# Kernel tuning notes

Hardware: AMD Instinct MI355X
Metric: run time of the kernel (lower is better)

Reference implementation:

```python
import jax, jax.numpy as jnp
import numpy as np

USER_NUM = 100000
ITEM_NUM = 50000
N_NODES = USER_NUM + ITEM_NUM
NNZ = 4800000
EMB = 64
N_LAYERS = 3
EPS = 0.2
NORM_EPS = 1e-12  # matches torch F.normalize eps clamp


def setup_inputs() -> dict:
    key = jax.random.key(0)
    ks = jax.random.split(key, 6)
    user_emb = jax.random.normal(ks[0], (USER_NUM, EMB), dtype=jnp.float32)
    item_emb = jax.random.normal(ks[1], (ITEM_NUM, EMB), dtype=jnp.float32)
    adj_rows = jax.random.randint(ks[2], (NNZ,), 0, N_NODES, dtype=jnp.int32)
    adj_cols = jax.random.randint(ks[3], (NNZ,), 0, N_NODES, dtype=jnp.int32)
    adj_vals = jax.random.uniform(ks[4], (NNZ,), dtype=jnp.float32)
    noise = jax.random.uniform(ks[5], (N_LAYERS, N_NODES, EMB), dtype=jnp.float32)
    return {"user_emb": user_emb, "item_emb": item_emb, "adj_rows": adj_rows,
            "adj_cols": adj_cols, "adj_vals": adj_vals, "noise": noise}


def reference(user_emb, item_emb, adj_rows, adj_cols, adj_vals, noise):
    # ego: [N, d]
    ego = jnp.concatenate([user_emb, item_emb], axis=0)

    def spmm(x):
        # sparse_norm_adj @ x via COO gather + segment-sum scatter
        return jax.ops.segment_sum(adj_vals[:, None] * x[adj_cols], adj_rows,
                                   num_segments=N_NODES)

    layer_outs = []
    for k in range(N_LAYERS):
        ego = spmm(ego)
        # perturbed=True branch: ego += sign(ego) * l2_normalize(noise) * eps
        r = noise[k]
        r_unit = r / jnp.maximum(jnp.linalg.norm(r, axis=-1, keepdims=True), NORM_EPS)
        ego = ego + jnp.sign(ego) * r_unit * EPS
        layer_outs.append(ego)

    all_emb = jnp.mean(jnp.stack(layer_outs, axis=1), axis=1)  # [N, d]
    return all_emb[:USER_NUM], all_emb[USER_NUM:]
```

## Files before the change

kernel.cpp:

```cpp
#include <hip/hip_runtime.h>

typedef unsigned int uint;

#define USER_NUM   100000
#define ITEM_NUM   50000
#define N_NODES    (USER_NUM + ITEM_NUM)
#define NNZ        4800000
#define EMB        64
#define EPS_F      0.2f
#define NORM_EPS_F 1e-12f

#define RB_SHIFT   8
#define RB         256
#define NB         ((N_NODES + RB - 1) / RB)
#define CAP        9216
#define BINA_CHUNK 4096
#define BINA_GRID  ((NNZ + BINA_CHUNK - 1) / BINA_CHUNK)
#define BB_K       9

__device__ inline float bflo(uint u) { return __uint_as_float(u << 16); }
__device__ inline float bfhi(uint u) { return __uint_as_float(u & 0xffff0000u); }
__device__ inline uint f2bf(float f) {
    uint u = __float_as_uint(f);
    return (u + 0x7fffu + ((u >> 16) & 1u)) >> 16;
}
__device__ inline uint pack2(float a, float b) { return f2bf(a) | (f2bf(b) << 16); }


__global__ void init_gcursor(int* __restrict__ g) {
    int b = blockIdx.x * blockDim.x + threadIdx.x;
    if (b < NB) g[b] = b * CAP;
}

__global__ __launch_bounds__(512) void binA_kernel(const int* __restrict__ rows,
                                                   const int* __restrict__ cols,
                                                   const float* __restrict__ vals,
                                                   int* __restrict__ gcursor,
                                                   int2* __restrict__ staging) {
    __shared__ int2 data[BINA_CHUNK];
    __shared__ unsigned short bid[BINA_CHUNK];
    __shared__ int hist[NB];
    __shared__ int rstart[NB + 1];
    __shared__ int gbase[NB];
    __shared__ int lcur[NB];
    __shared__ int wsum[8];
    int t = threadIdx.x;
    int cbeg = blockIdx.x * BINA_CHUNK;
    int cend = min(cbeg + BINA_CHUNK, NNZ);
    int total = cend - cbeg;

    int r[8], c[8];
    float v[8];
    if (t < NB) hist[t] = 0;
    if (t + 512 < NB) hist[t + 512] = 0;
    __syncthreads();
#pragma unroll
    for (int k = 0; k < 8; ++k) {
        int i = cbeg + (k << 9) + t;
        bool ok = i < cend;
        r[k] = ok ? rows[i] : -1;
        c[k] = ok ? cols[i] : 0;
        v[k] = ok ? vals[i] : 0.f;
    }
#pragma unroll
    for (int k = 0; k < 8; ++k)
        if (r[k] >= 0) atomicAdd(&hist[r[k] >> RB_SHIFT], 1);
    __syncthreads();

    int v0 = (2 * t < NB) ? hist[2 * t] : 0;
    int v1 = (2 * t + 1 < NB) ? hist[2 * t + 1] : 0;
    int pv = v0 + v1;
    int sc = pv;
#pragma unroll
    for (int off = 1; off < 64; off <<= 1) {
        int u = __shfl_up(sc, off, 64);
        if ((t & 63) >= off) sc += u;
    }
    if ((t & 63) == 63) wsum[t >> 6] = sc;
    __syncthreads();
    if (t < 64) {
        int ws = (t < 8) ? wsum[t] : 0;
#pragma unroll
        for (int off = 1; off < 8; off <<= 1) {
            int u = __shfl_up(ws, off, 64);
            if (t >= off) ws += u;
        }
        if (t < 8) wsum[t] = ws;
    }
    __syncthreads();
    int wid = t >> 6;
    int ex = sc - pv + ((wid > 0) ? wsum[wid - 1] : 0);
    if (2 * t <= NB) rstart[2 * t] = ex;
    if (2 * t + 1 <= NB) rstart[2 * t + 1] = ex + v0;
    if (2 * t < NB) { gbase[2 * t] = atomicAdd(&gcursor[2 * t], v0); lcur[2 * t] = 0; }
    if (2 * t + 1 < NB) { gbase[2 * t + 1] = atomicAdd(&gcursor[2 * t + 1], v1); lcur[2 * t + 1] = 0; }
    __syncthreads();

#pragma unroll
    for (int k = 0; k < 8; ++k) {
        if (r[k] >= 0) {
            int b = r[k] >> RB_SHIFT;
            int pos = rstart[b] + atomicAdd(&lcur[b], 1);
            data[pos] = make_int2(((r[k] & (RB - 1)) << 18) | c[k],
                                  __float_as_int(v[k]));
            bid[pos] = (unsigned short)b;
        }
    }
    __syncthreads();

    for (int i = t; i < total; i += 512) {
        int b = bid[i];
        staging[(long)gbase[b] + (i - rstart[b])] = data[i];
    }
}

__global__ __launch_bounds__(1024) void bscan_kernel(const int* __restrict__ gcursor,
                                                     int* __restrict__ bucket_base,
                                                     int* __restrict__ row_ptr) {
    __shared__ int wsum[16];
    int t = threadIdx.x;
    int c = (t < NB) ? (gcursor[t] - t * CAP) : 0;
    int sc = c;
#pragma unroll
    for (int off = 1; off < 64; off <<= 1) {
        int u = __shfl_up(sc, off, 64);
        if ((t & 63) >= off) sc += u;
    }
    if ((t & 63) == 63) wsum[t >> 6] = sc;
    __syncthreads();
    if (t < 64) {
        int ws = (t < 16) ? wsum[t] : 0;
#pragma unroll
        for (int off = 1; off < 16; off <<= 1) {
            int u = __shfl_up(ws, off, 64);
            if (t >= off) ws += u;
        }
        if (t < 16) wsum[t] = ws;
    }
    __syncthreads();
    int wid = t >> 6;
    int excl = sc - c + ((wid > 0) ? wsum[wid - 1] : 0);
    if (t < NB) bucket_base[t] = excl;
    if (t == 0) row_ptr[N_NODES] = NNZ;
}

__global__ __launch_bounds__(1024) void binB_kernel(const int* __restrict__ gcursor,
                                                    const int* __restrict__ bucket_base,
                                                    const int2* __restrict__ staging,
                                                    int2* __restrict__ edges,
                                                    int* __restrict__ row_ptr) {
    __shared__ int2 sorted[CAP];
    __shared__ int s[RB];
    __shared__ int cur[RB];
    __shared__ int wsum[16];
    int b = blockIdx.x;
    int t = threadIdx.x;
    int cnt = gcursor[b] - b * CAP;
    long sbase = (long)b * CAP;
    int base = bucket_base[b];

    int2 e[BB_K];
    if (t < RB) s[t] = 0;
    __syncthreads();
#pragma unroll
    for (int k = 0; k < BB_K; ++k) {
        int i = (k << 10) + t;
        e[k] = (i < cnt) ? staging[sbase + i] : make_int2(-1, 0);
    }
#pragma unroll
    for (int k = 0; k < BB_K; ++k)
        if (e[k].x >= 0) atomicAdd(&s[((unsigned)e[k].x) >> 18], 1);
    __syncthreads();

    int v = (t < RB) ? s[t] : 0;
    int sc = v;
#pragma unroll
    for (int off = 1; off < 64; off <<= 1) {
        int u = __shfl_up(sc, off, 64);
        if ((t & 63) >= off) sc += u;
    }
    if ((t & 63) == 63) wsum[t >> 6] = sc;
    __syncthreads();
    if (t < 64) {
        int ws = (t < 16) ? wsum[t] : 0;
#pragma unroll
        for (int off = 1; off < 16; off <<= 1) {
            int u = __shfl_up(ws, off, 64);
            if (t >= off) ws += u;
        }
        if (t < 16) wsum[t] = ws;
    }
    __syncthreads();
    int wid = t >> 6;
    int excl = sc - v + ((wid > 0) ? wsum[wid - 1] : 0);

    int row = (b << RB_SHIFT) + t;
    if (t < RB) {
        if (row < N_NODES) row_ptr[row] = base + excl;
        cur[t] = excl;
    }
    __syncthreads();
#pragma unroll
    for (int k = 0; k < BB_K; ++k) {
        if (e[k].x >= 0) {
            int rl = ((unsigned)e[k].x) >> 18;
            int pos = atomicAdd(&cur[rl], 1);
            sorted[pos] = make_int2(e[k].x & ((1 << 18) - 1), e[k].y);
        }
    }
    __syncthreads();
    for (int i = t; i < cnt; i += 1024)
        edges[base + i] = sorted[i];
}

__global__ void convert_kernel(const float4* __restrict__ u, const float4* __restrict__ it,
                               uint2* __restrict__ xh) {
    const int NU4 = USER_NUM * EMB / 4;
    const int NT4 = N_NODES * EMB / 4;
    int i = blockIdx.x * blockDim.x + threadIdx.x;
    int stride = gridDim.x * blockDim.x;
    for (; i < NT4; i += stride) {
        float4 f = (i < NU4) ? u[i] : it[i - NU4];
        xh[i] = make_uint2(pack2(f.x, f.y), pack2(f.z, f.w));
    }
}

__global__ __launch_bounds__(256) void spmm_layer_kernel(const uint* __restrict__ x,
                                                         uint* __restrict__ x_out,
                                                         const int* __restrict__ row_ptr,
                                                         const int2* __restrict__ edges,
                                                         const float* __restrict__ noise_k,
                                                         float* __restrict__ out, int mode) {
    int lane = threadIdx.x & 63;
    int row = blockIdx.x * 4 + (threadIdx.x >> 6);
    if (row >= N_NODES) return;
    int g = lane >> 3;
    int sub = lane & 7;

    int beg = row_ptr[row];
    int end = row_ptr[row + 1];
    int lim = end - 1;

    float a0 = 0.f, a1 = 0.f, a2 = 0.f, a3 = 0.f;
    float a4 = 0.f, a5 = 0.f, a6 = 0.f, a7 = 0.f;

    for (int base = beg; base < end; base += 16) {
        int i0 = base + g, i1 = base + 8 + g;
        int2 e0 = edges[min(i0, lim)];
        int2 e1 = edges[min(i1, lim)];
        const uint4* q0 = (const uint4*)(x + (long)e0.x * (EMB / 2));
        const uint4* q1 = (const uint4*)(x + (long)e1.x * (EMB / 2));
        uint4 h0 = q0[sub];
        uint4 h1 = q1[sub];
        float w0 = (i0 < end) ? __int_as_float(e0.y) : 0.f;
        float w1 = (i1 < end) ? __int_as_float(e1.y) : 0.f;
        a0 += w0 * bflo(h0.x); a1 += w0 * bfhi(h0.x);
        a2 += w0 * bflo(h0.y); a3 += w0 * bfhi(h0.y);
        a4 += w0 * bflo(h0.z); a5 += w0 * bfhi(h0.z);
        a6 += w0 * bflo(h0.w); a7 += w0 * bfhi(h0.w);
        a0 += w1 * bflo(h1.x); a1 += w1 * bfhi(h1.x);
        a2 += w1 * bflo(h1.y); a3 += w1 * bfhi(h1.y);
        a4 += w1 * bflo(h1.z); a5 += w1 * bfhi(h1.z);
        a6 += w1 * bflo(h1.w); a7 += w1 * bfhi(h1.w);
    }

#pragma unroll
    for (int off = 8; off <= 32; off <<= 1) {
        a0 += __shfl_xor(a0, off, 64); a1 += __shfl_xor(a1, off, 64);
        a2 += __shfl_xor(a2, off, 64); a3 += __shfl_xor(a3, off, 64);
        a4 += __shfl_xor(a4, off, 64); a5 += __shfl_xor(a5, off, 64);
        a6 += __shfl_xor(a6, off, 64); a7 += __shfl_xor(a7, off, 64);
    }

    const float4* nz = (const float4*)(noise_k + (long)row * EMB);
    float4 n0 = nz[sub * 2];
    float4 n1 = nz[sub * 2 + 1];
    float ss = n0.x * n0.x + n0.y * n0.y + n0.z * n0.z + n0.w * n0.w
             + n1.x * n1.x + n1.y * n1.y + n1.z * n1.z + n1.w * n1.w;
    ss += __shfl_xor(ss, 1, 64);
    ss += __shfl_xor(ss, 2, 64);
    ss += __shfl_xor(ss, 4, 64);
    float s = EPS_F / fmaxf(sqrtf(ss), NORM_EPS_F);

    float v0 = a0 + ((a0 > 0.f) ? 1.f : ((a0 < 0.f) ? -1.f : 0.f)) * n0.x * s;
    float v1 = a1 + ((a1 > 0.f) ? 1.f : ((a1 < 0.f) ? -1.f : 0.f)) * n0.y * s;
    float v2 = a2 + ((a2 > 0.f) ? 1.f : ((a2 < 0.f) ? -1.f : 0.f)) * n0.z * s;
    float v3 = a3 + ((a3 > 0.f) ? 1.f : ((a3 < 0.f) ? -1.f : 0.f)) * n0.w * s;
    float v4 = a4 + ((a4 > 0.f) ? 1.f : ((a4 < 0.f) ? -1.f : 0.f)) * n1.x * s;
    float v5 = a5 + ((a5 > 0.f) ? 1.f : ((a5 < 0.f) ? -1.f : 0.f)) * n1.y * s;
    float v6 = a6 + ((a6 > 0.f) ? 1.f : ((a6 < 0.f) ? -1.f : 0.f)) * n1.z * s;
    float v7 = a7 + ((a7 > 0.f) ? 1.f : ((a7 < 0.f) ? -1.f : 0.f)) * n1.w * s;

    if (g == 0) {
        float4* po = (float4*)(out + (long)row * EMB);
        float4 f01 = make_float4(v0, v1, v2, v3);
        float4 f23 = make_float4(v4, v5, v6, v7);
        if (mode == 0) {
            po[sub * 2] = f01;
            po[sub * 2 + 1] = f23;
        } else if (mode == 1) {
            float4 o0 = po[sub * 2], o1 = po[sub * 2 + 1];
            o0.x += v0; o0.y += v1; o0.z += v2; o0.w += v3;
            o1.x += v4; o1.y += v5; o1.z += v6; o1.w += v7;
            po[sub * 2] = o0;
            po[sub * 2 + 1] = o1;
        } else {
            float4 o0 = po[sub * 2], o1 = po[sub * 2 + 1];
            o0.x = (o0.x + v0) * (1.f / 3.f); o0.y = (o0.y + v1) * (1.f / 3.f);
            o0.z = (o0.z + v2) * (1.f / 3.f); o0.w = (o0.w + v3) * (1.f / 3.f);
            o1.x = (o1.x + v4) * (1.f / 3.f); o1.y = (o1.y + v5) * (1.f / 3.f);
            o1.z = (o1.z + v6) * (1.f / 3.f); o1.w = (o1.w + v7) * (1.f / 3.f);
            po[sub * 2] = o0;
            po[sub * 2 + 1] = o1;
        }
        if (mode != 2) {
            uint4* ph = (uint4*)(x_out + (long)row * (EMB / 2));
            ph[sub] = make_uint4(pack2(v0, v1), pack2(v2, v3),
                                 pack2(v4, v5), pack2(v6, v7));
        }
    }
}


extern "C" void kernel_launch(void* const* d_in, const int* in_sizes, int n_in,
                              void* d_out, int out_size, void* d_ws, size_t ws_size,
                              hipStream_t stream) {
    const float* user_emb = (const float*)d_in[0];
    const float* item_emb = (const float*)d_in[1];
    const int*   adj_rows = (const int*)d_in[2];
    const int*   adj_cols = (const int*)d_in[3];
    const float* adj_vals = (const float*)d_in[4];
    const float* noise    = (const float*)d_in[5];
    float* out = (float*)d_out;

    char* ws = (char*)d_ws;
    size_t off = 0;
    auto alloc = [&](size_t bytes) {
        char* p = ws + off;
        off += (bytes + 15) & ~size_t(15);
        return p;
    };
    int*   row_ptr     = (int*)alloc((N_NODES + 1) * sizeof(int));
    int*   gcursor     = (int*)alloc(NB * sizeof(int));
    int*   bucket_base = (int*)alloc(NB * sizeof(int));
    int2*  edges       = (int2*)alloc((size_t)NNZ * sizeof(int2));
    int2*  staging     = (int2*)alloc((size_t)NB * CAP * sizeof(int2));
    uint* xh_a = (uint*)staging;
    uint* xh_b = (uint*)((char*)staging + (size_t)N_NODES * EMB * 2);

    init_gcursor<<<3, 256, 0, stream>>>(gcursor);
    binA_kernel<<<BINA_GRID, 512, 0, stream>>>(adj_rows, adj_cols, adj_vals,
                                               gcursor, staging);
    bscan_kernel<<<1, 1024, 0, stream>>>(gcursor, bucket_base, row_ptr);
    binB_kernel<<<NB, 1024, 0, stream>>>(gcursor, bucket_base, staging, edges,
                                         row_ptr);

    convert_kernel<<<2048, 256, 0, stream>>>((const float4*)user_emb,
                                             (const float4*)item_emb, (uint2*)xh_a);

    const int LGRID = (N_NODES + 3) / 4;
    const size_t NE = (size_t)N_NODES * EMB;
    spmm_layer_kernel<<<LGRID, 256, 0, stream>>>(xh_a, xh_b, row_ptr, edges,
                                                 noise + 0 * NE, out, 0);
    spmm_layer_kernel<<<LGRID, 256, 0, stream>>>(xh_b, xh_a, row_ptr, edges,
                                                 noise + 1 * NE, out, 1);
    spmm_layer_kernel<<<LGRID, 256, 0, stream>>>(xh_a, nullptr, row_ptr, edges,
                                                 noise + 2 * NE, out, 2);
}
```

Baseline: 750.2 us.

## Fuse three SpMM layers into persistent kernel with grid barrier; merge prep kernels

Replaces the three per-layer SpMM launches with one persistent kernel of 1792 blocks that loops over rows and layers, separated by a software grid barrier built from striped atomic counters. It also folds the fp32-to-bf16 conversion into binA, moves the bucket prefix scan into each binB block, and replaces init_gcursor with a memset of per-bucket counts. The aim is to cut kernel launches and tail gaps between layers, at the cost of relying on all 1792 blocks being co-resident (deadlock risk otherwise) and losing the one-row-per-wave dynamic scheduling.

```diff
diff --git a/kernel.cpp b/kernel.cpp
--- a/kernel.cpp
+++ b/kernel.cpp
@@ -1,6 +1,7 @@
 #include <hip/hip_runtime.h>
 
 typedef unsigned int uint;
+typedef unsigned long long ull;
 
 #define USER_NUM   100000
 #define ITEM_NUM   50000
@@ -18,6 +19,10 @@
 #define BINA_GRID  ((NNZ + BINA_CHUNK - 1) / BINA_CHUNK)
 #define BB_K       9
 
+#define SPMM_BLOCKS 1792
+#define SPMM_WAVES  (SPMM_BLOCKS * 4)
+#define BAR_STRIDE  256
+
 __device__ inline float bflo(uint u) { return __uint_as_float(u << 16); }
 __device__ inline float bfhi(uint u) { return __uint_as_float(u & 0xffff0000u); }
 __device__ inline uint f2bf(float f) {
@@ -27,16 +32,14 @@
 __device__ inline uint pack2(float a, float b) { return f2bf(a) | (f2bf(b) << 16); }
 
 
-__global__ void init_gcursor(int* __restrict__ g) {
-    int b = blockIdx.x * blockDim.x + threadIdx.x;
-    if (b < NB) g[b] = b * CAP;
-}
-
 __global__ __launch_bounds__(512) void binA_kernel(const int* __restrict__ rows,
                                                    const int* __restrict__ cols,
                                                    const float* __restrict__ vals,
-                                                   int* __restrict__ gcursor,
-                                                   int2* __restrict__ staging) {
+                                                   int* __restrict__ gcount,
+                                                   int2* __restrict__ staging,
+                                                   const float4* __restrict__ uemb,
+                                                   const float4* __restrict__ iemb,
+                                                   uint2* __restrict__ xh) {
     __shared__ int2 data[BINA_CHUNK];
     __shared__ unsigned short bid[BINA_CHUNK];
     __shared__ int hist[NB];
@@ -92,8 +95,14 @@
     int ex = sc - pv + ((wid > 0) ? wsum[wid - 1] : 0);
     if (2 * t <= NB) rstart[2 * t] = ex;
     if (2 * t + 1 <= NB) rstart[2 * t + 1] = ex + v0;
-    if (2 * t < NB) { gbase[2 * t] = atomicAdd(&gcursor[2 * t], v0); lcur[2 * t] = 0; }
-    if (2 * t + 1 < NB) { gbase[2 * t + 1] = atomicAdd(&gcursor[2 * t + 1], v1); lcur[2 * t + 1] = 0; }
+    if (2 * t < NB) {
+        gbase[2 * t] = (2 * t) * CAP + atomicAdd(&gcount[2 * t], v0);
+        lcur[2 * t] = 0;
+    }
+    if (2 * t + 1 < NB) {
+        gbase[2 * t + 1] = (2 * t + 1) * CAP + atomicAdd(&gcount[2 * t + 1], v1);
+        lcur[2 * t + 1] = 0;
+    }
     __syncthreads();
 
 #pragma unroll
@@ -112,40 +121,17 @@
         int b = bid[i];
         staging[(long)gbase[b] + (i - rstart[b])] = data[i];
     }
-}
-
-__global__ __launch_bounds__(1024) void bscan_kernel(const int* __restrict__ gcursor,
-                                                     int* __restrict__ bucket_base,
-                                                     int* __restrict__ row_ptr) {
-    __shared__ int wsum[16];
-    int t = threadIdx.x;
-    int c = (t < NB) ? (gcursor[t] - t * CAP) : 0;
-    int sc = c;
-#pragma unroll
-    for (int off = 1; off < 64; off <<= 1) {
-        int u = __shfl_up(sc, off, 64);
-        if ((t & 63) >= off) sc += u;
-    }
-    if ((t & 63) == 63) wsum[t >> 6] = sc;
-    __syncthreads();
-    if (t < 64) {
-        int ws = (t < 16) ? wsum[t] : 0;
-#pragma unroll
-        for (int off = 1; off < 16; off <<= 1) {
-            int u = __shfl_up(ws, off, 64);
-            if (t >= off) ws += u;
-        }
-        if (t < 16) wsum[t] = ws;
-    }
-    __syncthreads();
-    int wid = t >> 6;
-    int excl = sc - c + ((wid > 0) ? wsum[wid - 1] : 0);
-    if (t < NB) bucket_base[t] = excl;
-    if (t == 0) row_ptr[N_NODES] = NNZ;
-}
-
-__global__ __launch_bounds__(1024) void binB_kernel(const int* __restrict__ gcursor,
-                                                    const int* __restrict__ bucket_base,
+
+    const int NU4 = USER_NUM * EMB / 4;
+    const int NT4 = N_NODES * EMB / 4;
+    int stride = gridDim.x * blockDim.x;
+    for (int i = blockIdx.x * blockDim.x + t; i < NT4; i += stride) {
+        float4 f = (i < NU4) ? uemb[i] : iemb[i - NU4];
+        xh[i] = make_uint2(pack2(f.x, f.y), pack2(f.z, f.w));
+    }
+}
+
+__global__ __launch_bounds__(1024) void binB_kernel(const int* __restrict__ gcount,
                                                     const int2* __restrict__ staging,
                                                     int2* __restrict__ edges,
                                                     int* __restrict__ row_ptr) {
@@ -153,27 +139,24 @@
     __shared__ int s[RB];
     __shared__ int cur[RB];
     __shared__ int wsum[16];
+    __shared__ int base_sh;
     int b = blockIdx.x;
     int t = threadIdx.x;
-    int cnt = gcursor[b] - b * CAP;
+    int cnt = gcount[b];
     long sbase = (long)b * CAP;
-    int base = bucket_base[b];
 
     int2 e[BB_K];
     if (t < RB) s[t] = 0;
-    __syncthreads();
 #pragma unroll
     for (int k = 0; k < BB_K; ++k) {
         int i = (k << 10) + t;
         e[k] = (i < cnt) ? staging[sbase + i] : make_int2(-1, 0);
     }
-#pragma unroll
-    for (int k = 0; k < BB_K; ++k)
-        if (e[k].x >= 0) atomicAdd(&s[((unsigned)e[k].x) >> 18], 1);
-    __syncthreads();
-
-    int v = (t < RB) ? s[t] : 0;
-    int sc = v;
+
+    int c0 = (2 * t < NB) ? gcount[2 * t] : 0;
+    int c1 = (2 * t + 1 < NB) ? gcount[2 * t + 1] : 0;
+    int pv = c0 + c1;
+    int sc = pv;
 #pragma unroll
     for (int off = 1; off < 64; off <<= 1) {
         int u = __shfl_up(sc, off, 64);
@@ -192,13 +175,44 @@
     }
     __syncthreads();
     int wid = t >> 6;
-    int excl = sc - v + ((wid > 0) ? wsum[wid - 1] : 0);
+    int ex = sc - pv + ((wid > 0) ? wsum[wid - 1] : 0);
+    if (2 * t == b) base_sh = ex;
+    if (2 * t + 1 == b) base_sh = ex + c0;
+
+#pragma unroll
+    for (int k = 0; k < BB_K; ++k)
+        if (e[k].x >= 0) atomicAdd(&s[((unsigned)e[k].x) >> 18], 1);
+    __syncthreads();
+    int base = base_sh;
+
+    int v = (t < RB) ? s[t] : 0;
+    int sc2 = v;
+#pragma unroll
+    for (int off = 1; off < 64; off <<= 1) {
+        int u = __shfl_up(sc2, off, 64);
+        if ((t & 63) >= off) sc2 += u;
+    }
+    if ((t & 63) == 63) wsum[t >> 6] = sc2;
+    __syncthreads();
+    if (t < 64) {
+        int ws = (t < 16) ? wsum[t] : 0;
+#pragma unroll
+        for (int off = 1; off < 16; off <<= 1) {
+            int u = __shfl_up(ws, off, 64);
+            if (t >= off) ws += u;
+        }
+        if (t < 16) wsum[t] = ws;
+    }
+    __syncthreads();
+    int wid2 = t >> 6;
+    int excl = sc2 - v + ((wid2 > 0) ? wsum[wid2 - 1] : 0);
 
     int row = (b << RB_SHIFT) + t;
     if (t < RB) {
         if (row < N_NODES) row_ptr[row] = base + excl;
         cur[t] = excl;
     }
+    if (b == NB - 1 && t == 0) row_ptr[N_NODES] = NNZ;
     __syncthreads();
 #pragma unroll
     for (int k = 0; k < BB_K; ++k) {
@@ -213,110 +227,127 @@
         edges[base + i] = sorted[i];
 }
 
-__global__ void convert_kernel(const float4* __restrict__ u, const float4* __restrict__ it,
-                               uint2* __restrict__ xh) {
-    const int NU4 = USER_NUM * EMB / 4;
-    const int NT4 = N_NODES * EMB / 4;
-    int i = blockIdx.x * blockDim.x + threadIdx.x;
-    int stride = gridDim.x * blockDim.x;
-    for (; i < NT4; i += stride) {
-        float4 f = (i < NU4) ? u[i] : it[i - NU4];
-        xh[i] = make_uint2(pack2(f.x, f.y), pack2(f.z, f.w));
-    }
-}
-
-__global__ __launch_bounds__(256) void spmm_layer_kernel(const uint* __restrict__ x,
-                                                         uint* __restrict__ x_out,
-                                                         const int* __restrict__ row_ptr,
-                                                         const int2* __restrict__ edges,
-                                                         const float* __restrict__ noise_k,
-                                                         float* __restrict__ out, int mode) {
+__global__ __launch_bounds__(256, 8) void spmm_fused(
+        uint* __restrict__ xh_a, uint* __restrict__ xh_b,
+        const int* __restrict__ row_ptr, const int2* __restrict__ edges,
+        const float* __restrict__ noise, float* __restrict__ out,
+        int* __restrict__ bar) {
     int lane = threadIdx.x & 63;
-    int row = blockIdx.x * 4 + (threadIdx.x >> 6);
-    if (row >= N_NODES) return;
+    int gw = blockIdx.x * 4 + (threadIdx.x >> 6);
     int g = lane >> 3;
     int sub = lane & 7;
 
-    int beg = row_ptr[row];
-    int end = row_ptr[row + 1];
-    int lim = end - 1;
-
-    float a0 = 0.f, a1 = 0.f, a2 = 0.f, a3 = 0.f;
-    float a4 = 0.f, a5 = 0.f, a6 = 0.f, a7 = 0.f;
-
-    for (int base = beg; base < end; base += 16) {
-        int i0 = base + g, i1 = base + 8 + g;
-        int2 e0 = edges[min(i0, lim)];
-        int2 e1 = edges[min(i1, lim)];
-        const uint4* q0 = (const uint4*)(x + (long)e0.x * (EMB / 2));
-        const uint4* q1 = (const uint4*)(x + (long)e1.x * (EMB / 2));
-        uint4 h0 = q0[sub];
-        uint4 h1 = q1[sub];
-        float w0 = (i0 < end) ? __int_as_float(e0.y) : 0.f;
-        float w1 = (i1 < end) ? __int_as_float(e1.y) : 0.f;
-        a0 += w0 * bflo(h0.x); a1 += w0 * bfhi(h0.x);
-        a2 += w0 * bflo(h0.y); a3 += w0 * bfhi(h0.y);
-        a4 += w0 * bflo(h0.z); a5 += w0 * bfhi(h0.z);
-        a6 += w0 * bflo(h0.w); a7 += w0 * bfhi(h0.w);
-        a0 += w1 * bflo(h1.x); a1 += w1 * bfhi(h1.x);
-        a2 += w1 * bflo(h1.y); a3 += w1 * bfhi(h1.y);
-        a4 += w1 * bflo(h1.z); a5 += w1 * bfhi(h1.z);
-        a6 += w1 * bflo(h1.w); a7 += w1 * bfhi(h1.w);
-    }
-
-#pragma unroll
-    for (int off = 8; off <= 32; off <<= 1) {
-        a0 += __shfl_xor(a0, off, 64); a1 += __shfl_xor(a1, off, 64);
-        a2 += __shfl_xor(a2, off, 64); a3 += __shfl_xor(a3, off, 64);
-        a4 += __shfl_xor(a4, off, 64); a5 += __shfl_xor(a5, off, 64);
-        a6 += __shfl_xor(a6, off, 64); a7 += __shfl_xor(a7, off, 64);
-    }
-
-    const float4* nz = (const float4*)(noise_k + (long)row * EMB);
-    float4 n0 = nz[sub * 2];
-    float4 n1 = nz[sub * 2 + 1];
-    float ss = n0.x * n0.x + n0.y * n0.y + n0.z * n0.z + n0.w * n0.w
-             + n1.x * n1.x + n1.y * n1.y + n1.z * n1.z + n1.w * n1.w;
-    ss += __shfl_xor(ss, 1, 64);
-    ss += __shfl_xor(ss, 2, 64);
-    ss += __shfl_xor(ss, 4, 64);
-    float s = EPS_F / fmaxf(sqrtf(ss), NORM_EPS_F);
-
-    float v0 = a0 + ((a0 > 0.f) ? 1.f : ((a0 < 0.f) ? -1.f : 0.f)) * n0.x * s;
-    float v1 = a1 + ((a1 > 0.f) ? 1.f : ((a1 < 0.f) ? -1.f : 0.f)) * n0.y * s;
-    float v2 = a2 + ((a2 > 0.f) ? 1.f : ((a2 < 0.f) ? -1.f : 0.f)) * n0.z * s;
-    float v3 = a3 + ((a3 > 0.f) ? 1.f : ((a3 < 0.f) ? -1.f : 0.f)) * n0.w * s;
-    float v4 = a4 + ((a4 > 0.f) ? 1.f : ((a4 < 0.f) ? -1.f : 0.f)) * n1.x * s;
-    float v5 = a5 + ((a5 > 0.f) ? 1.f : ((a5 < 0.f) ? -1.f : 0.f)) * n1.y * s;
-    float v6 = a6 + ((a6 > 0.f) ? 1.f : ((a6 < 0.f) ? -1.f : 0.f)) * n1.z * s;
-    float v7 = a7 + ((a7 > 0.f) ? 1.f : ((a7 < 0.f) ? -1.f : 0.f)) * n1.w * s;
-
-    if (g == 0) {
-        float4* po = (float4*)(out + (long)row * EMB);
-        float4 f01 = make_float4(v0, v1, v2, v3);
-        float4 f23 = make_float4(v4, v5, v6, v7);
-        if (mode == 0) {
-            po[sub * 2] = f01;
-            po[sub * 2 + 1] = f23;
-        } else if (mode == 1) {
-            float4 o0 = po[sub * 2], o1 = po[sub * 2 + 1];
-            o0.x += v0; o0.y += v1; o0.z += v2; o0.w += v3;
-            o1.x += v4; o1.y += v5; o1.z += v6; o1.w += v7;
-            po[sub * 2] = o0;
-            po[sub * 2 + 1] = o1;
-        } else {
-            float4 o0 = po[sub * 2], o1 = po[sub * 2 + 1];
-            o0.x = (o0.x + v0) * (1.f / 3.f); o0.y = (o0.y + v1) * (1.f / 3.f);
-            o0.z = (o0.z + v2) * (1.f / 3.f); o0.w = (o0.w + v3) * (1.f / 3.f);
-            o1.x = (o1.x + v4) * (1.f / 3.f); o1.y = (o1.y + v5) * (1.f / 3.f);
-            o1.z = (o1.z + v6) * (1.f / 3.f); o1.w = (o1.w + v7) * (1.f / 3.f);
-            po[sub * 2] = o0;
-            po[sub * 2 + 1] = o1;
-        }
-        if (mode != 2) {
-            uint4* ph = (uint4*)(x_out + (long)row * (EMB / 2));
-            ph[sub] = make_uint4(pack2(v0, v1), pack2(v2, v3),
-                                 pack2(v4, v5), pack2(v6, v7));
+    const uint* xs = xh_a;
+    uint* xd = xh_b;
+
+#pragma unroll
+    for (int layer = 0; layer < 3; ++layer) {
+        const float* noise_k = noise + (size_t)layer * N_NODES * EMB;
+        for (int row = gw; row < N_NODES; row += SPMM_WAVES) {
+            int beg = row_ptr[row];
+            int end = row_ptr[row + 1];
+            int lim = end - 1;
+
+            float a0 = 0.f, a1 = 0.f, a2 = 0.f, a3 = 0.f;
+            float a4 = 0.f, a5 = 0.f, a6 = 0.f, a7 = 0.f;
+
+            for (int base = beg; base < end; base += 16) {
+                int i0 = base + g, i1 = base + 8 + g;
+                int2 e0 = edges[min(i0, lim)];
+                int2 e1 = edges[min(i1, lim)];
+                const uint4* q0 = (const uint4*)(xs + (long)e0.x * (EMB / 2));
+                const uint4* q1 = (const uint4*)(xs + (long)e1.x * (EMB / 2));
+                uint4 h0 = q0[sub];
+                uint4 h1 = q1[sub];
+                float w0 = (i0 < end) ? __int_as_float(e0.y) : 0.f;
+                float w1 = (i1 < end) ? __int_as_float(e1.y) : 0.f;
+                a0 += w0 * bflo(h0.x); a1 += w0 * bfhi(h0.x);
+                a2 += w0 * bflo(h0.y); a3 += w0 * bfhi(h0.y);
+                a4 += w0 * bflo(h0.z); a5 += w0 * bfhi(h0.z);
+                a6 += w0 * bflo(h0.w); a7 += w0 * bfhi(h0.w);
+                a0 += w1 * bflo(h1.x); a1 += w1 * bfhi(h1.x);
+                a2 += w1 * bflo(h1.y); a3 += w1 * bfhi(h1.y);
+                a4 += w1 * bflo(h1.z); a5 += w1 * bfhi(h1.z);
+                a6 += w1 * bflo(h1.w); a7 += w1 * bfhi(h1.w);
+            }
+
+#pragma unroll
+            for (int off = 8; off <= 32; off <<= 1) {
+                a0 += __shfl_xor(a0, off, 64); a1 += __shfl_xor(a1, off, 64);
+                a2 += __shfl_xor(a2, off, 64); a3 += __shfl_xor(a3, off, 64);
+                a4 += __shfl_xor(a4, off, 64); a5 += __shfl_xor(a5, off, 64);
+                a6 += __shfl_xor(a6, off, 64); a7 += __shfl_xor(a7, off, 64);
+            }
+
+            const float4* nz = (const float4*)(noise_k + (long)row * EMB);
+            float4 n0 = nz[sub * 2];
+            float4 n1 = nz[sub * 2 + 1];
+            float ss = n0.x * n0.x + n0.y * n0.y + n0.z * n0.z + n0.w * n0.w
+                     + n1.x * n1.x + n1.y * n1.y + n1.z * n1.z + n1.w * n1.w;
+            ss += __shfl_xor(ss, 1, 64);
+            ss += __shfl_xor(ss, 2, 64);
+            ss += __shfl_xor(ss, 4, 64);
+            float s = EPS_F / fmaxf(sqrtf(ss), NORM_EPS_F);
+
+            float v0 = a0 + ((a0 > 0.f) ? 1.f : ((a0 < 0.f) ? -1.f : 0.f)) * n0.x * s;
+            float v1 = a1 + ((a1 > 0.f) ? 1.f : ((a1 < 0.f) ? -1.f : 0.f)) * n0.y * s;
+            float v2 = a2 + ((a2 > 0.f) ? 1.f : ((a2 < 0.f) ? -1.f : 0.f)) * n0.z * s;
+            float v3 = a3 + ((a3 > 0.f) ? 1.f : ((a3 < 0.f) ? -1.f : 0.f)) * n0.w * s;
+            float v4 = a4 + ((a4 > 0.f) ? 1.f : ((a4 < 0.f) ? -1.f : 0.f)) * n1.x * s;
+            float v5 = a5 + ((a5 > 0.f) ? 1.f : ((a5 < 0.f) ? -1.f : 0.f)) * n1.y * s;
+            float v6 = a6 + ((a6 > 0.f) ? 1.f : ((a6 < 0.f) ? -1.f : 0.f)) * n1.z * s;
+            float v7 = a7 + ((a7 > 0.f) ? 1.f : ((a7 < 0.f) ? -1.f : 0.f)) * n1.w * s;
+
+            if (g == 0) {
+                float4* po = (float4*)(out + (long)row * EMB);
+                if (layer == 0) {
+                    po[sub * 2] = make_float4(v0, v1, v2, v3);
+                    po[sub * 2 + 1] = make_float4(v4, v5, v6, v7);
+                } else if (layer == 1) {
+                    float4 o0 = po[sub * 2], o1 = po[sub * 2 + 1];
+                    o0.x += v0; o0.y += v1; o0.z += v2; o0.w += v3;
+                    o1.x += v4; o1.y += v5; o1.z += v6; o1.w += v7;
+                    po[sub * 2] = o0;
+                    po[sub * 2 + 1] = o1;
+                } else {
+                    float4 o0 = po[sub * 2], o1 = po[sub * 2 + 1];
+                    o0.x = (o0.x + v0) * (1.f / 3.f); o0.y = (o0.y + v1) * (1.f / 3.f);
+                    o0.z = (o0.z + v2) * (1.f / 3.f); o0.w = (o0.w + v3) * (1.f / 3.f);
+                    o1.x = (o1.x + v4) * (1.f / 3.f); o1.y = (o1.y + v5) * (1.f / 3.f);
+                    o1.z = (o1.z + v6) * (1.f / 3.f); o1.w = (o1.w + v7) * (1.f / 3.f);
+                    po[sub * 2] = o0;
+                    po[sub * 2 + 1] = o1;
+                }
+                if (layer != 2) {
+                    uint4* ph = (uint4*)(xd + (long)row * (EMB / 2));
+                    ph[sub] = make_uint4(pack2(v0, v1), pack2(v2, v3),
+                                         pack2(v4, v5), pack2(v6, v7));
+                }
+            }
+        }
+
+        if (layer < 2) {
+            __syncthreads();
+            if (threadIdx.x == 0) {
+                __threadfence();
+                int* bb = bar + layer * BAR_STRIDE;
+                __hip_atomic_fetch_add(&bb[(blockIdx.x & 15) << 4], 1,
+                                       __ATOMIC_RELEASE, __HIP_MEMORY_SCOPE_AGENT);
+                for (;;) {
+                    int ssum = 0;
+#pragma unroll
+                    for (int k = 0; k < 16; ++k)
+                        ssum += __hip_atomic_load(&bb[k << 4], __ATOMIC_ACQUIRE,
+                                                  __HIP_MEMORY_SCOPE_AGENT);
+                    if (ssum >= SPMM_BLOCKS) break;
+                    __builtin_amdgcn_s_sleep(8);
+                }
+                __threadfence();
+            }
+            __syncthreads();
+            const uint* tmp = xs;
+            xs = xd;
+            xd = (uint*)tmp;
         }
     }
 }
@@ -340,30 +371,25 @@
         off += (bytes + 15) & ~size_t(15);
         return p;
     };
-    int*   row_ptr     = (int*)alloc((N_NODES + 1) * sizeof(int));
-    int*   gcursor     = (int*)alloc(NB * sizeof(int));
-    int*   bucket_base = (int*)alloc(NB * sizeof(int));
-    int2*  edges       = (int2*)alloc((size_t)NNZ * sizeof(int2));
-    int2*  staging     = (int2*)alloc((size_t)NB * CAP * sizeof(int2));
-    uint* xh_a = (uint*)staging;
-    uint* xh_b = (uint*)((char*)staging + (size_t)N_NODES * EMB * 2);
-
-    init_gcursor<<<3, 256, 0, stream>>>(gcursor);
+    int*   row_ptr = (int*)alloc((N_NODES + 1) * sizeof(int));
+    int*   ctrl    = (int*)alloc((NB + 2 * BAR_STRIDE) * sizeof(int));
+    int2*  edges   = (int2*)alloc((size_t)NNZ * sizeof(int2));
+    uint*  xh_a    = (uint*)alloc((size_t)N_NODES * EMB * 2);
+    int2*  staging = (int2*)alloc((size_t)NB * CAP * sizeof(int2));
+    uint* xh_b = (uint*)staging;
+
+    int* gcount = ctrl;
+    int* bar    = ctrl + NB;
+
+    hipMemsetAsync(ctrl, 0, (NB + 2 * BAR_STRIDE) * sizeof(int), stream);
+
     binA_kernel<<<BINA_GRID, 512, 0, stream>>>(adj_rows, adj_cols, adj_vals,
-                                               gcursor, staging);
-    bscan_kernel<<<1, 1024, 0, stream>>>(gcursor, bucket_base, row_ptr);
-    binB_kernel<<<NB, 1024, 0, stream>>>(gcursor, bucket_base, staging, edges,
-                                         row_ptr);
-
-    convert_kernel<<<2048, 256, 0, stream>>>((const float4*)user_emb,
-                                             (const float4*)item_emb, (uint2*)xh_a);
-
-    const int LGRID = (N_NODES + 3) / 4;
-    const size_t NE = (size_t)N_NODES * EMB;
-    spmm_layer_kernel<<<LGRID, 256, 0, stream>>>(xh_a, xh_b, row_ptr, edges,
-                                                 noise + 0 * NE, out, 0);
-    spmm_layer_kernel<<<LGRID, 256, 0, stream>>>(xh_b, xh_a, row_ptr, edges,
-                                                 noise + 1 * NE, out, 1);
-    spmm_layer_kernel<<<LGRID, 256, 0, stream>>>(xh_a, nullptr, row_ptr, edges,
-                                                 noise + 2 * NE, out, 2);
-}
+                                               gcount, staging,
+                                               (const float4*)user_emb,
+                                               (const float4*)item_emb,
+                                               (uint2*)xh_a);
+    binB_kernel<<<NB, 1024, 0, stream>>>(gcount, staging, edges, row_ptr);
+
+    spmm_fused<<<SPMM_BLOCKS, 256, 0, stream>>>(xh_a, xh_b, row_ptr, edges,
+                                                noise, out, bar);
+}
```

New measurement: 2.062 ms. 175% more time.
